# Kernel tuning notes

Hardware: AMD Instinct MI355X
Metric: run time of the kernel (lower is better)

## Reference

```python
import jax, jax.numpy as jnp
import numpy as np

B, L, V, E, H, DH, M, NL, BS, NR = 4, 2048, 32000, 512, 8, 64, 2048, 4, 64, 3
NEG = -1e9


def _sinusoidal_pe(length, dim):
    # LRA common_layers sinusoidal init: first half sin, second half cos.
    pos = np.arange(length, dtype=np.float32)[:, None]
    half = dim // 2
    div = np.exp(np.arange(half, dtype=np.float32) * -(np.log(10000.0) / half))
    pe = np.zeros((length, dim), np.float32)
    pe[:, :half] = np.sin(pos * div)
    pe[:, half:2 * half] = np.cos(pos * div)
    return jnp.asarray(pe)


def _bigbird_block_mask(seq_len, block_size, num_rand, seed):
    # BigBird sparsity at block granularity: window(3-band) + global(first/last
    # block rows & cols) + num_rand random blocks per row (connectivity_seed).
    nb = seq_len // block_size
    m = np.zeros((nb, nb), dtype=bool)
    for i in range(nb):
        for d in (-1, 0, 1):
            j = i + d
            if 0 <= j < nb:
                m[i, j] = True
    m[0, :] = True
    m[-1, :] = True
    m[:, 0] = True
    m[:, -1] = True
    rng = np.random.RandomState(seed)
    for i in range(1, nb - 1):
        avoid = {0, nb - 1, i - 1, i, i + 1}
        cand = np.array([j for j in range(nb) if j not in avoid])
        pick = rng.permutation(cand)[:num_rand]
        m[i, pick] = True
    return jnp.asarray(np.kron(m, np.ones((block_size, block_size), dtype=bool)))


_SPARSE_MASKS = [_bigbird_block_mask(L, BS, NR, lyr) for lyr in range(NL)]  # [L,L] bool per layer
_PE = _sinusoidal_pe(L, E)


def _ln(x, scale, bias, eps=1e-6):
    mu = jnp.mean(x, axis=-1, keepdims=True)
    var = jnp.mean(jnp.square(x - mu), axis=-1, keepdims=True)
    return (x - mu) * jax.lax.rsqrt(var + eps) * scale + bias


def setup_inputs() -> dict:
    key = jax.random.key(0)
    ks = jax.random.split(key, 12)
    s_qkv = 1.0 / np.sqrt(E)
    s_mlp = 1.0 / np.sqrt(E)
    return {
        "tokens": jax.random.randint(ks[0], (B, L), 0, V, dtype=jnp.int32),
        "embed": jax.random.normal(ks[1], (V, E), jnp.float32),
        "ln1_s": jnp.ones((NL, E), jnp.float32),
        "ln1_b": jnp.zeros((NL, E), jnp.float32),
        "wq": jax.random.normal(ks[2], (NL, E, H, DH), jnp.float32) * s_qkv,
        "wk": jax.random.normal(ks[3], (NL, E, H, DH), jnp.float32) * s_qkv,
        "wv": jax.random.normal(ks[4], (NL, E, H, DH), jnp.float32) * s_qkv,
        "wo": jax.random.normal(ks[5], (NL, H, DH, E), jnp.float32) * s_qkv,
        "ln2_s": jnp.ones((NL, E), jnp.float32),
        "ln2_b": jnp.zeros((NL, E), jnp.float32),
        "w1": jax.random.normal(ks[6], (NL, E, M), jnp.float32) * s_mlp,
        "b1": jnp.zeros((NL, M), jnp.float32),
        "w2": jax.random.normal(ks[7], (NL, M, E), jnp.float32) * (1.0 / np.sqrt(M)),
        "b2": jnp.zeros((NL, E), jnp.float32),
        "lnf_s": jnp.ones((E,), jnp.float32),
        "lnf_b": jnp.zeros((E,), jnp.float32),
    }


def reference(tokens, embed, ln1_s, ln1_b, wq, wk, wv, wo,
              ln2_s, ln2_b, w1, b1, w2, b2, lnf_s, lnf_b):
    pad = tokens > 0                                  # [B,L]
    x = embed[tokens] + _PE[None]                     # [B,L,E]
    scale = 1.0 / jnp.sqrt(jnp.asarray(DH, x.dtype))
    for lyr in range(NL):
        y = _ln(x, ln1_s[lyr], ln1_b[lyr])
        q = jnp.einsum("ble,ehd->blhd", y, wq[lyr]) * scale
        k = jnp.einsum("ble,ehd->blhd", y, wk[lyr])
        v = jnp.einsum("ble,ehd->blhd", y, wv[lyr])
        scores = jnp.einsum("blhd,bmhd->bhlm", q, k)  # [B,H,L,L]
        mask = (_SPARSE_MASKS[lyr][None, None]
                & pad[:, None, :, None] & pad[:, None, None, :])
        probs = jax.nn.softmax(jnp.where(mask, scores, NEG), axis=-1)
        o = jnp.einsum("bhlm,bmhd->blhd", probs, v)
        x = x + jnp.einsum("blhd,hde->ble", o, wo[lyr])
        y = _ln(x, ln2_s[lyr], ln2_b[lyr])
        h = jax.nn.gelu(jnp.einsum("ble,em->blm", y, w1[lyr]) + b1[lyr])
        x = x + jnp.einsum("blm,me->ble", h, w2[lyr]) + b2[lyr]
    return _ln(x, lnf_s, lnf_b)
```

## Files before the change

### kernel.cpp

```cpp
#include <hip/hip_runtime.h>
#include <hip/hip_bf16.h>
#include <cmath>
#include <cstdint>
#include <cstddef>

#define B_   4
#define L_   2048
#define E_   512
#define H_   8
#define DH_  64
#define M_   2048
#define NL_  4
#define NB_  32
#define BS_  64
#define CH_  12

typedef short bf16x8 __attribute__((ext_vector_type(8)));
typedef short bf16x4 __attribute__((ext_vector_type(4)));
typedef float f32x4 __attribute__((ext_vector_type(4)));

__device__ __forceinline__ short f2bf(float f) {
    union { __hip_bfloat16 h; short s; } u;
    u.h = __float2bfloat16(f);
    return u.s;
}
__device__ __forceinline__ float bf2f(short s) {
    union { short s; __hip_bfloat16 h; } u;
    u.s = s;
    return __bfloat162float(u.h);
}

struct MaskTable { unsigned m[NL_][NB_]; };
struct CxMT { unsigned key[624]; int pos; };

constexpr unsigned cx_next(CxMT& st) {
    if (st.pos >= 624) {
        for (int i = 0; i < 624; ++i) {
            unsigned y = (st.key[i] & 0x80000000u) | (st.key[(i + 1) % 624] & 0x7fffffffu);
            st.key[i] = st.key[(i + 397) % 624] ^ (y >> 1) ^ ((y & 1u) ? 0x9908b0dfu : 0u);
        }
        st.pos = 0;
    }
    unsigned y = st.key[st.pos++];
    y ^= y >> 11;
    y ^= (y << 7) & 0x9d2c5680u;
    y ^= (y << 15) & 0xefc60000u;
    y ^= y >> 18;
    return y;
}
constexpr unsigned cx_interval(CxMT& st, unsigned maxv) {
    if (maxv == 0u) return 0u;
    unsigned mask = maxv;
    mask |= mask >> 1; mask |= mask >> 2; mask |= mask >> 4;
    mask |= mask >> 8; mask |= mask >> 16;
    unsigned v = cx_next(st) & mask;
    while (v > maxv) v = cx_next(st) & mask;
    return v;
}
constexpr MaskTable compute_masks() {
    MaskTable T{};
    for (int lyr = 0; lyr < NL_; ++lyr) {
        unsigned m[NB_] = {};
        for (int i = 0; i < NB_; ++i) {
            unsigned w = 1u << i;
            if (i > 0) w |= 1u << (i - 1);
            if (i < NB_ - 1) w |= 1u << (i + 1);
            w |= 1u | (1u << (NB_ - 1));
            m[i] = w;
        }
        m[0] = 0xffffffffu;
        m[NB_ - 1] = 0xffffffffu;
        CxMT st{};
        unsigned s = (unsigned)lyr;
        for (int i = 0; i < 624; ++i) {
            st.key[i] = s;
            s = 1812433253u * (s ^ (s >> 30)) + (unsigned)i + 1u;
        }
        st.pos = 624;
        for (int i = 1; i < NB_ - 1; ++i) {
            int cand[NB_] = {};
            int n = 0;
            for (int j = 0; j < NB_; ++j) {
                if (j == 0 || j == NB_ - 1 || j == i - 1 || j == i || j == i + 1) continue;
                cand[n++] = j;
            }
            for (int kk = n - 1; kk >= 1; --kk) {
                int jj = (int)cx_interval(st, (unsigned)kk);
                int tmp = cand[kk]; cand[kk] = cand[jj]; cand[jj] = tmp;
            }
            m[i] |= (1u << cand[0]) | (1u << cand[1]) | (1u << cand[2]);
        }
        for (int i = 0; i < NB_; ++i) T.m[lyr][i] = m[i];
    }
    return T;
}

struct WorkTable {
    int n_items[NL_];
    int n_cmb[NL_];
    unsigned char itm_qb[NL_][40];
    unsigned char itm_j0[NL_][40];
    unsigned char itm_jn[NL_][40];
    unsigned char itm_slot[NL_][40];
    unsigned char cmb_qb[NL_][8];
    unsigned char cmb_slot0[NL_][8];
    unsigned char cmb_nch[NL_][8];
    unsigned char jlist[NL_][NB_][NB_];
};

constexpr WorkTable compute_work() {
    WorkTable T{};
    MaskTable M = compute_masks();
    for (int lyr = 0; lyr < NL_; ++lyr) {
        int items = 0, slots = 0, ncmb = 0;
        for (int qb = 0; qb < NB_; ++qb) {
            int cnt = 0;
            for (int j = 0; j < NB_; ++j)
                if ((M.m[lyr][qb] >> j) & 1u)
                    T.jlist[lyr][qb][cnt++] = (unsigned char)j;
            int nch = (cnt + CH_ - 1) / CH_;
            if (nch == 1) {
                T.itm_qb[lyr][items] = (unsigned char)qb;
                T.itm_j0[lyr][items] = 0;
                T.itm_jn[lyr][items] = (unsigned char)cnt;
                T.itm_slot[lyr][items] = 0xFF;
                items++;
            } else {
                T.cmb_qb[lyr][ncmb] = (unsigned char)qb;
                T.cmb_slot0[lyr][ncmb] = (unsigned char)slots;
                T.cmb_nch[lyr][ncmb] = (unsigned char)nch;
                ncmb++;
                int base = cnt / nch, rem = cnt % nch, off = 0;
                for (int c = 0; c < nch; ++c) {
                    int cl = base + (c < rem ? 1 : 0);
                    T.itm_qb[lyr][items] = (unsigned char)qb;
                    T.itm_j0[lyr][items] = (unsigned char)off;
                    T.itm_jn[lyr][items] = (unsigned char)cl;
                    T.itm_slot[lyr][items] = (unsigned char)slots;
                    items++; slots++; off += cl;
                }
            }
        }
        T.n_items[lyr] = items;
        T.n_cmb[lyr] = ncmb;
    }
    return T;
}

static constexpr WorkTable WT_HOST = compute_work();
__constant__ WorkTable g_wt = compute_work();

__global__ __launch_bounds__(256) void embed_kernel(const int* __restrict__ tokens,
                                                    const float* __restrict__ embed,
                                                    float* __restrict__ x) {
    int idx = blockIdx.x * 256 + threadIdx.x;
    int l = idx >> 6;
    int e0 = (idx & 63) * 8;
    float pe[8];
    #pragma unroll
    for (int j = 0; j < 8; ++j) {
        int e = e0 + j;
        int jj = e & 255;
        float div = expf((float)jj * -0.03597789207717895f);
        float arg = (float)l * div;
        pe[j] = (e < 256) ? sinf(arg) : cosf(arg);
    }
    #pragma unroll
    for (int b = 0; b < B_; ++b) {
        int tok = tokens[b * L_ + l];
        const float* em = embed + (size_t)tok * E_ + e0;
        f32x4 v0 = *(const f32x4*)em;
        f32x4 v1 = *(const f32x4*)(em + 4);
        #pragma unroll
        for (int j = 0; j < 4; ++j) { v0[j] += pe[j]; v1[j] += pe[4 + j]; }
        float* xo = x + ((size_t)(b * L_ + l)) * E_ + e0;
        *(f32x4*)xo = v0;
        *(f32x4*)(xo + 4) = v1;
    }
}

template<int OUTBF>
__global__ __launch_bounds__(256) void ln_kernel(const float* __restrict__ x,
                                                 const float* __restrict__ gamma,
                                                 const float* __restrict__ beta,
                                                 void* __restrict__ yout) {
    int t = threadIdx.x;
    int lane = t & 63;
    int row = blockIdx.x * 4 + (t >> 6);
    const float* xr = x + (size_t)row * E_ + lane * 8;
    f32x4 a0 = *(const f32x4*)xr;
    f32x4 a1 = *(const f32x4*)(xr + 4);
    float s = a0[0] + a0[1] + a0[2] + a0[3] + a1[0] + a1[1] + a1[2] + a1[3];
    #pragma unroll
    for (int off = 1; off < 64; off <<= 1) s += __shfl_xor(s, off, 64);
    float mu = s * (1.0f / E_);
    float q = 0.0f;
    #pragma unroll
    for (int j = 0; j < 4; ++j) { float d = a0[j] - mu; q += d * d; }
    #pragma unroll
    for (int j = 0; j < 4; ++j) { float d = a1[j] - mu; q += d * d; }
    #pragma unroll
    for (int off = 1; off < 64; off <<= 1) q += __shfl_xor(q, off, 64);
    float rstd = rsqrtf(q * (1.0f / E_) + 1e-6f);
    f32x4 g0 = *(const f32x4*)(gamma + lane * 8);
    f32x4 g1 = *(const f32x4*)(gamma + lane * 8 + 4);
    f32x4 b0 = *(const f32x4*)(beta + lane * 8);
    f32x4 b1 = *(const f32x4*)(beta + lane * 8 + 4);
    float o[8];
    #pragma unroll
    for (int j = 0; j < 4; ++j) o[j] = (a0[j] - mu) * rstd * g0[j] + b0[j];
    #pragma unroll
    for (int j = 0; j < 4; ++j) o[4 + j] = (a1[j] - mu) * rstd * g1[j] + b1[j];
    if (OUTBF) {
        bf16x8 pk;
        #pragma unroll
        for (int j = 0; j < 8; ++j) pk[j] = f2bf(o[j]);
        *(bf16x8*)((short*)yout + (size_t)row * E_ + lane * 8) = pk;
    } else {
        float* yr = (float*)yout + (size_t)row * E_ + lane * 8;
        *(f32x4*)yr = f32x4{o[0], o[1], o[2], o[3]};
        *(f32x4*)(yr + 4) = f32x4{o[4], o[5], o[6], o[7]};
    }
}

__global__ __launch_bounds__(256) void convT_kernel(const float* __restrict__ W,
                                                    short* __restrict__ Wt,
                                                    int K, int N,
                                                    size_t wStride, size_t wtStride,
                                                    float scale) {
    __shared__ float Ts[64][65];
    const float* Wl = W + blockIdx.z * wStride;
    short* Wtl = Wt + blockIdx.z * wtStride;
    int n0 = blockIdx.x * 64, k0 = blockIdx.y * 64;
    int t = threadIdx.x;
    int c = t & 63, r0 = t >> 6;
    #pragma unroll
    for (int i = 0; i < 16; ++i) {
        int r = r0 * 16 + i;
        Ts[r][c] = Wl[(size_t)(k0 + r) * N + n0 + c] * scale;
    }
    __syncthreads();
    #pragma unroll
    for (int i = 0; i < 16; ++i) {
        int r = r0 * 16 + i;
        Wtl[(size_t)(n0 + r) * K + k0 + c] = f2bf(Ts[c][r]);
    }
}

__device__ __forceinline__ float gelu_tanh(float x) {
    float u = x * (1.5957691216057308f + 0.07135480122394604f * x * x);
    return x / (1.0f + __expf(-u));
}

template<int BM, int BN, int ACT, int OUTBF>
__global__ __launch_bounds__(512) void mgemm_kernel(const short* __restrict__ A,
                                                    const short* __restrict__ Bt,
                                                    const float* __restrict__ bias,
                                                    const float* __restrict__ res,
                                                    void* __restrict__ Cout,
                                                    int M, int N, int K) {
    constexpr int WR = 2, WC = 4;
    constexpr int FM = BM / WR / 16;
    constexpr int FN = BN / WC / 16;
    constexpr int ASZ = BM * 64;
    constexpr int BSZ = BN * 64;
    constexpr int PAD = 8;
    constexpr int CW = BN + PAD;
    static_assert((size_t)(OUTBF ? BM * CW * 2 : BM * CW * 4) <= (size_t)2 * (ASZ + BSZ) * 2,
                  "epilogue stage must fit in dbuf LDS");
    __shared__ __align__(16) short smem[2 * (ASZ + BSZ)];

    int t = threadIdx.x;
    int w = t >> 6, l = t & 63;
    int l15 = l & 15, lg = l >> 4;
    int wr = w >> 2, wc = w & 3;
    int rowbase = wr * (BM / WR), colbase = wc * (BN / WC);

    int nwg = (int)(gridDim.x * gridDim.y);
    int orig = (int)(blockIdx.y * gridDim.x + blockIdx.x);
    int sid = (orig & 7) * (nwg >> 3) + (orig >> 3);
    int bx = sid % (int)gridDim.x, by = sid / (int)gridDim.x;
    int brow = by * BM, bcol = bx * BN;

    int swz = ((t & 7) ^ ((t >> 3) & 7)) * 8;
    f32x4 acc[FM][FN] = {};

    const int nt = K >> 6;

    auto stage = [&](int buf, int k0) {
        short* Ad = smem + buf * ASZ;
        short* Bd = smem + 2 * ASZ + buf * BSZ;
        #pragma unroll
        for (int it = 0; it < BM / 64; ++it) {
            int row = it * 64 + (t >> 3);
            const short* ga = A + (size_t)(brow + row) * K + k0 + swz;
            __builtin_amdgcn_global_load_lds(
                (const __attribute__((address_space(1))) unsigned int*)ga,
                (__attribute__((address_space(3))) unsigned int*)(Ad + (it * 64 + w * 8) * 64),
                16, 0, 0);
        }
        #pragma unroll
        for (int it = 0; it < BN / 64; ++it) {
            int row = it * 64 + (t >> 3);
            const short* gb = Bt + (size_t)(bcol + row) * K + k0 + swz;
            __builtin_amdgcn_global_load_lds(
                (const __attribute__((address_space(1))) unsigned int*)gb,
                (__attribute__((address_space(3))) unsigned int*)(Bd + (it * 64 + w * 8) * 64),
                16, 0, 0);
        }
    };

    stage(0, 0);
    asm volatile("s_waitcnt vmcnt(0)" ::: "memory");
    __builtin_amdgcn_s_barrier();

    int cur = 0;
    for (int kt = 0; kt < nt; ++kt) {
        if (kt + 1 < nt) stage(cur ^ 1, (kt + 1) << 6);
        const short* Ar = smem + cur * ASZ;
        const short* Br = smem + 2 * ASZ + cur * BSZ;
        #pragma unroll
        for (int kk = 0; kk < 64; kk += 32) {
            bf16x8 af[FM], bfr[FN];
            #pragma unroll
            for (int m = 0; m < FM; ++m)
                af[m] = *(const bf16x8*)(Ar + (rowbase + m * 16 + l15) * 64
                                            + (((kk >> 3) + lg) ^ (l15 & 7)) * 8);
            #pragma unroll
            for (int n = 0; n < FN; ++n)
                bfr[n] = *(const bf16x8*)(Br + (colbase + n * 16 + l15) * 64
                                             + (((kk >> 3) + lg) ^ (l15 & 7)) * 8);
            #pragma unroll
            for (int m = 0; m < FM; ++m)
                #pragma unroll
                for (int n = 0; n < FN; ++n)
                    acc[m][n] = __builtin_amdgcn_mfma_f32_16x16x32_bf16(af[m], bfr[n], acc[m][n], 0, 0, 0);
        }
        asm volatile("s_waitcnt vmcnt(0) lgkmcnt(0)" ::: "memory");
        __builtin_amdgcn_s_barrier();
        cur ^= 1;
    }

    if (OUTBF) {
        short* Cs = smem;
        #pragma unroll
        for (int m = 0; m < FM; ++m) {
            int row = rowbase + m * 16 + lg * 4;
            #pragma unroll
            for (int n = 0; n < FN; ++n) {
                int col = colbase + n * 16 + l15;
                float bv = bias ? bias[bcol + col] : 0.0f;
                #pragma unroll
                for (int r = 0; r < 4; ++r) {
                    float vv = acc[m][n][r] + bv;
                    if (ACT == 1) vv = gelu_tanh(vv);
                    Cs[(row + r) * CW + col] = f2bf(vv);
                }
            }
        }
        __syncthreads();
        #pragma unroll
        for (int it = 0; it < BM * BN / 8 / 512; ++it) {
            int c = it * 512 + t;
            int row = c / (BN / 8), c8 = c % (BN / 8);
            *(bf16x8*)((short*)Cout + (size_t)(brow + row) * N + bcol + c8 * 8) =
                *(const bf16x8*)(Cs + row * CW + c8 * 8);
        }
    } else {
        float* Cs = (float*)smem;
        #pragma unroll
        for (int m = 0; m < FM; ++m) {
            int row = rowbase + m * 16 + lg * 4;
            #pragma unroll
            for (int n = 0; n < FN; ++n) {
                int col = colbase + n * 16 + l15;
                float bv = bias ? bias[bcol + col] : 0.0f;
                #pragma unroll
                for (int r = 0; r < 4; ++r)
                    Cs[(row + r) * CW + col] = acc[m][n][r] + bv;
            }
        }
        __syncthreads();
        #pragma unroll
        for (int it = 0; it < BM * BN / 4 / 512; ++it) {
            int c = it * 512 + t;
            int row = c / (BN / 4), c4 = c % (BN / 4);
            f32x4 vv = *(const f32x4*)(Cs + row * CW + c4 * 4);
            size_t gi = (size_t)(brow + row) * N + bcol + c4 * 4;
            if (res) vv += *(const f32x4*)(res + gi);
            *(f32x4*)((float*)Cout + gi) = vv;
        }
    }
}

#define KSTR 72

__global__ __launch_bounds__(256) void attn_kernel(const short* __restrict__ qkv,
                                                   const int* __restrict__ tokens,
                                                   short* __restrict__ o,
                                                   float* __restrict__ pacc,
                                                   float* __restrict__ pm,
                                                   float* __restrict__ pl,
                                                   int lyr) {
    __shared__ __align__(16) short Ks[64][KSTR];
    __shared__ __align__(16) short Vt[64][KSTR];
    __shared__ __align__(16) short Pw[4][16][KSTR];
    __shared__ unsigned long long qbits_s;
    __shared__ unsigned long long kbits_s;

    int item = blockIdx.x, h = blockIdx.y, b = blockIdx.z;
    int qb   = g_wt.itm_qb[lyr][item];
    int j0   = g_wt.itm_j0[lyr][item];
    int jn   = g_wt.itm_jn[lyr][item];
    int slot = g_wt.itm_slot[lyr][item];
    const unsigned char* jl = g_wt.jlist[lyr][qb];

    int t = threadIdx.x;
    int l = t & 63, w = t >> 6;
    int l15 = l & 15, lg = l >> 4;
    int srow = t >> 3, sdb = t & 7;

    if (t < 64) {
        unsigned long long qm = __ballot(tokens[b * L_ + qb * 64 + t] > 0);
        if (t == 0) qbits_s = qm;
    }

    int qrow = qb * 64 + w * 16 + l15;
    const short* qp = qkv + (size_t)(b * L_ + qrow) * 1536 + h * 64;
    bf16x8 qf0 = *(const bf16x8*)(qp + lg * 8);
    bf16x8 qf1 = *(const bf16x8*)(qp + lg * 8 + 32);

    f32x4 acc[4] = {};
    float m_r = -INFINITY, l_r = 0.0f;

    bf16x8 kr0, kr1, vr0, vr1;
    int pn = 0;
    auto LOAD = [&](int ci) {
        int jb = jl[j0 + ci];
        const short* base = qkv + (size_t)(b * L_ + jb * 64 + srow) * 1536 + h * 64;
        kr0 = *(const bf16x8*)(base + 512 + sdb * 8);
        kr1 = *(const bf16x8*)(base + (size_t)32 * 1536 + 512 + sdb * 8);
        vr0 = *(const bf16x8*)(base + 1024 + sdb * 8);
        vr1 = *(const bf16x8*)(base + (size_t)32 * 1536 + 1024 + sdb * 8);
        if (t < 64) pn = tokens[b * L_ + jb * 64 + t];
    };
    LOAD(0);

    for (int ci = 0; ci < jn; ++ci) {
        __syncthreads();
        *(bf16x8*)&Ks[srow][sdb * 8] = kr0;
        *(bf16x8*)&Ks[srow + 32][sdb * 8] = kr1;
        #pragma unroll
        for (int j = 0; j < 8; ++j) {
            Vt[sdb * 8 + j][(srow & 7) + 8 * ((srow >> 3) ^ sdb)] = vr0[j];
            Vt[sdb * 8 + j][(srow & 7) + 8 * (((srow >> 3) + 4) ^ sdb)] = vr1[j];
        }
        if (t < 64) {
            unsigned long long km = __ballot(pn > 0);
            if (t == 0) kbits_s = km;
        }
        __syncthreads();

        if (ci + 1 < jn) LOAD(ci + 1);

        f32x4 sacc[4];
        __builtin_amdgcn_s_setprio(1);
        #pragma unroll
        for (int f = 0; f < 4; ++f) {
            bf16x8 kk0 = *(const bf16x8*)&Ks[16 * f + l15][lg * 8];
            bf16x8 kk1 = *(const bf16x8*)&Ks[16 * f + l15][lg * 8 + 32];
            f32x4 z = {};
            z = __builtin_amdgcn_mfma_f32_16x16x32_bf16(kk0, qf0, z, 0, 0, 0);
            z = __builtin_amdgcn_mfma_f32_16x16x32_bf16(kk1, qf1, z, 0, 0, 0);
            sacc[f] = z;
        }
        __builtin_amdgcn_s_setprio(0);

        unsigned long long kb = kbits_s;
        bool pq = (qbits_s >> (w * 16 + l15)) & 1ull;
        unsigned vm = 0;
        #pragma unroll
        for (int f = 0; f < 4; ++f)
            vm |= ((unsigned)(kb >> (16 * f + 4 * lg)) & 0xFu) << (4 * f);
        if (!pq) vm = 0;

        float mx = -INFINITY;
        #pragma unroll
        for (int f = 0; f < 4; ++f)
            #pragma unroll
            for (int r = 0; r < 4; ++r)
                if ((vm >> (4 * f + r)) & 1u) mx = fmaxf(mx, sacc[f][r]);
        mx = fmaxf(mx, __shfl_xor(mx, 16, 64));
        mx = fmaxf(mx, __shfl_xor(mx, 32, 64));
        float nm = fmaxf(m_r, mx);

        float pv[16];
        float sum = 0.0f;
        #pragma unroll
        for (int f = 0; f < 4; ++f)
            #pragma unroll
            for (int r = 0; r < 4; ++r) {
                float p = ((vm >> (4 * f + r)) & 1u) ? __expf(sacc[f][r] - nm) : 0.0f;
                pv[4 * f + r] = p;
                sum += p;
            }
        sum += __shfl_xor(sum, 16, 64);
        sum += __shfl_xor(sum, 32, 64);
        float al = (nm == -INFINITY) ? 1.0f : __expf(m_r - nm);
        m_r = nm;
        l_r = l_r * al + sum;

        #pragma unroll
        for (int f = 0; f < 4; ++f) {
            bf16x4 pk;
            #pragma unroll
            for (int r = 0; r < 4; ++r) pk[r] = f2bf(pv[4 * f + r]);
            *(bf16x4*)&Pw[w][l15][16 * f + 4 * lg] = pk;
        }

        float alr[4];
        #pragma unroll
        for (int r = 0; r < 4; ++r) alr[r] = __shfl(al, lg * 4 + r, 64);
        #pragma unroll
        for (int fd = 0; fd < 4; ++fd)
            #pragma unroll
            for (int r = 0; r < 4; ++r) acc[fd][r] *= alr[r];

        bf16x8 pa0 = *(const bf16x8*)&Pw[w][l15][lg * 8];
        bf16x8 pa1 = *(const bf16x8*)&Pw[w][l15][lg * 8 + 32];
        __builtin_amdgcn_s_setprio(1);
        #pragma unroll
        for (int fd = 0; fd < 4; ++fd) {
            int dd = 16 * fd + l15;
            bf16x8 vv0 = *(const bf16x8*)&Vt[dd][8 * (lg ^ (dd >> 3))];
            bf16x8 vv1 = *(const bf16x8*)&Vt[dd][8 * ((4 + lg) ^ (dd >> 3))];
            acc[fd] = __builtin_amdgcn_mfma_f32_16x16x32_bf16(pa0, vv0, acc[fd], 0, 0, 0);
            acc[fd] = __builtin_amdgcn_mfma_f32_16x16x32_bf16(pa1, vv1, acc[fd], 0, 0, 0);
        }
        __builtin_amdgcn_s_setprio(0);
    }

    float lrr[4], mrr[4];
    #pragma unroll
    for (int r = 0; r < 4; ++r) {
        lrr[r] = __shfl(l_r, lg * 4 + r, 64);
        mrr[r] = __shfl(m_r, lg * 4 + r, 64);
    }
    unsigned long long qbits = qbits_s;

    if (slot == 0xFF) {
        #pragma unroll
        for (int r = 0; r < 4; ++r) {
            int rw = lg * 4 + r;
            int gl = qb * 64 + w * 16 + rw;
            size_t ob = (size_t)(b * L_ + gl) * 512 + h * 64 + l15;
            bool ok = ((qbits >> (w * 16 + rw)) & 1ull) && (lrr[r] > 0.0f);
            if (ok) {
                float inv = 1.0f / lrr[r];
                #pragma unroll
                for (int fd = 0; fd < 4; ++fd) o[ob + 16 * fd] = f2bf(acc[fd][r] * inv);
            } else {
                #pragma unroll
                for (int fd = 0; fd < 4; ++fd) {
                    float s = 0.0f;
                    for (int m = 0; m < L_; ++m)
                        s += bf2f(qkv[(size_t)(b * L_ + m) * 1536 + 1024 + h * 64 + 16 * fd + l15]);
                    o[ob + 16 * fd] = f2bf(s * (1.0f / L_));
                }
            }
        }
    } else {
        size_t pb = ((size_t)slot * B_ + b) * H_ + h;
        #pragma unroll
        for (int r = 0; r < 4; ++r) {
            int rloc = w * 16 + lg * 4 + r;
            #pragma unroll
            for (int fd = 0; fd < 4; ++fd)
                pacc[pb * 4096 + (size_t)rloc * 64 + 16 * fd + l15] = acc[fd][r];
            if (l15 == 0) {
                pm[pb * 64 + rloc] = mrr[r];
                pl[pb * 64 + rloc] = lrr[r];
            }
        }
    }
}

__global__ __launch_bounds__(256) void attn_combine(const short* __restrict__ qkv,
                                                    const int* __restrict__ tokens,
                                                    short* __restrict__ o,
                                                    const float* __restrict__ pacc,
                                                    const float* __restrict__ pm,
                                                    const float* __restrict__ pl,
                                                    int lyr) {
    int ci = blockIdx.x, h = blockIdx.y, b = blockIdx.z;
    int qb  = g_wt.cmb_qb[lyr][ci];
    int s0  = g_wt.cmb_slot0[lyr][ci];
    int nch = g_wt.cmb_nch[lyr][ci];
    int t = threadIdx.x;
    int r = t >> 2, dq = t & 3;
    int grow = qb * 64 + r;
    bool pq = tokens[b * L_ + grow] > 0;
    float M = -INFINITY;
    for (int c = 0; c < nch; ++c)
        M = fmaxf(M, pm[(((size_t)(s0 + c) * B_ + b) * H_ + h) * 64 + r]);
    size_t ob = (size_t)(b * L_ + grow) * 512 + h * 64 + dq * 16;
    if (pq && M > -1e30f) {
        float lsum = 0.0f;
        float accd[16] = {};
        for (int c = 0; c < nch; ++c) {
            size_t pb = ((size_t)(s0 + c) * B_ + b) * H_ + h;
            float wgt = __expf(pm[pb * 64 + r] - M);
            lsum += pl[pb * 64 + r] * wgt;
            const float* pa = pacc + pb * 4096 + (size_t)r * 64 + dq * 16;
            #pragma unroll
            for (int j = 0; j < 16; ++j) accd[j] += pa[j] * wgt;
        }
        float inv = 1.0f / lsum;
        #pragma unroll
        for (int j = 0; j < 16; ++j) o[ob + j] = f2bf(accd[j] * inv);
    } else {
        #pragma unroll
        for (int j = 0; j < 16; ++j) {
            float s = 0.0f;
            for (int m = 0; m < L_; ++m)
                s += bf2f(qkv[(size_t)(b * L_ + m) * 1536 + 1024 + h * 64 + dq * 16 + j]);
            o[ob + j] = f2bf(s * (1.0f / L_));
        }
    }
}

extern "C" void kernel_launch(void* const* d_in, const int* in_sizes, int n_in,
                              void* d_out, int out_size, void* d_ws, size_t ws_size,
                              hipStream_t stream) {
    (void)in_sizes; (void)n_in; (void)out_size; (void)ws_size;
    const int*   tokens = (const int*)d_in[0];
    const float* embed  = (const float*)d_in[1];
    const float* ln1_s  = (const float*)d_in[2];
    const float* ln1_b  = (const float*)d_in[3];
    const float* wq     = (const float*)d_in[4];
    const float* wk     = (const float*)d_in[5];
    const float* wv     = (const float*)d_in[6];
    const float* wo     = (const float*)d_in[7];
    const float* ln2_s  = (const float*)d_in[8];
    const float* ln2_b  = (const float*)d_in[9];
    const float* w1     = (const float*)d_in[10];
    const float* b1     = (const float*)d_in[11];
    const float* w2     = (const float*)d_in[12];
    const float* b2     = (const float*)d_in[13];
    const float* lnf_s  = (const float*)d_in[14];
    const float* lnf_b  = (const float*)d_in[15];
    float* out = (float*)d_out;

    const size_t BLE = (size_t)B_ * L_ * E_;
    char* ws = (char*)d_ws;
    float* x    = (float*)ws;
    short* yb   = (short*)(x + BLE);
    short* R    = yb + BLE;
    short* qkv  = R;
    short* ob   = R + 3 * BLE;
    short* hb   = R;
    short* qkvt = R + 4 * BLE;
    short* wot  = qkvt + (size_t)NL_ * 1536 * 512;
    short* w1t  = wot + (size_t)NL_ * 512 * 512;
    short* w2t  = w1t + (size_t)NL_ * 2048 * 512;
    float* pacc = (float*)(w2t + (size_t)NL_ * 512 * 2048);
    float* pm   = pacc + (size_t)8 * B_ * H_ * 4096;
    float* pl   = pm + (size_t)8 * B_ * H_ * 64;

    convT_kernel<<<dim3(8, 8, NL_), 256, 0, stream>>>(wq, qkvt,          512, 512, 262144, 786432, 0.125f);
    convT_kernel<<<dim3(8, 8, NL_), 256, 0, stream>>>(wk, qkvt + 262144, 512, 512, 262144, 786432, 1.0f);
    convT_kernel<<<dim3(8, 8, NL_), 256, 0, stream>>>(wv, qkvt + 524288, 512, 512, 262144, 786432, 1.0f);
    convT_kernel<<<dim3(8, 8, NL_), 256, 0, stream>>>(wo, wot,           512, 512, 262144, 262144, 1.0f);
    convT_kernel<<<dim3(32, 8, NL_), 256, 0, stream>>>(w1, w1t,          512, 2048, 1048576, 1048576, 1.0f);
    convT_kernel<<<dim3(8, 32, NL_), 256, 0, stream>>>(w2, w2t,          2048, 512, 1048576, 1048576, 1.0f);

    embed_kernel<<<(L_ * E_ / 8) / 256, 256, 0, stream>>>(tokens, embed, x);

    const int MR = B_ * L_;
    const int LNG = MR / 4;
    for (int lyr = 0; lyr < NL_; ++lyr) {
        ln_kernel<1><<<LNG, 256, 0, stream>>>(x, ln1_s + lyr * E_, ln1_b + lyr * E_, yb);
        mgemm_kernel<128, 128, 0, 1><<<dim3(12, 64), 512, 0, stream>>>(
            yb, qkvt + (size_t)lyr * 786432, nullptr, nullptr, qkv, MR, 1536, 512);
        attn_kernel<<<dim3(WT_HOST.n_items[lyr], H_, B_), 256, 0, stream>>>(
            qkv, tokens, ob, pacc, pm, pl, lyr);
        attn_combine<<<dim3(WT_HOST.n_cmb[lyr], H_, B_), 256, 0, stream>>>(
            qkv, tokens, ob, pacc, pm, pl, lyr);
        mgemm_kernel<64, 128, 0, 0><<<dim3(4, 128), 512, 0, stream>>>(
            ob, wot + (size_t)lyr * 262144, nullptr, x, x, MR, 512, 512);
        ln_kernel<1><<<LNG, 256, 0, stream>>>(x, ln2_s + lyr * E_, ln2_b + lyr * E_, yb);
        mgemm_kernel<128, 128, 1, 1><<<dim3(16, 64), 512, 0, stream>>>(
            yb, w1t + (size_t)lyr * 1048576, b1 + (size_t)lyr * M_, nullptr, hb, MR, 2048, 512);
        mgemm_kernel<64, 128, 0, 0><<<dim3(4, 128), 512, 0, stream>>>(
            hb, w2t + (size_t)lyr * 1048576, b2 + (size_t)lyr * E_, x, x, MR, 512, 2048);
    }
    ln_kernel<0><<<LNG, 256, 0, stream>>>(x, lnf_s, lnf_b, out);
}
```

Baseline: 602.3 us.

## Double-buffer K/V shared tiles in sparse attention and shrink key chunk size

The attention kernel now keeps two LDS buffers for K, V and the key pad bits. The next block is stored into the spare buffer after the current compute, so each iteration needs one barrier instead of two, and global loads are issued two blocks ahead. The key-chunk size CH_ drops from 12 to 8, which splits query rows into more work items and raises grid parallelism, at the cost of more partial-result combining. LDS use roughly doubles for K/V, which may lower occupancy.

New measurement: 594.5 us. No clear change (-1.3%).

```diff
diff --git a/kernel.cpp b/kernel.cpp
--- a/kernel.cpp
+++ b/kernel.cpp
@@ -13,7 +13,7 @@
 #define NL_  4
 #define NB_  32
 #define BS_  64
-#define CH_  12
+#define CH_  8
 
 typedef short bf16x8 __attribute__((ext_vector_type(8)));
 typedef short bf16x4 __attribute__((ext_vector_type(4)));
@@ -98,10 +98,10 @@
 struct WorkTable {
     int n_items[NL_];
     int n_cmb[NL_];
-    unsigned char itm_qb[NL_][40];
-    unsigned char itm_j0[NL_][40];
-    unsigned char itm_jn[NL_][40];
-    unsigned char itm_slot[NL_][40];
+    unsigned char itm_qb[NL_][48];
+    unsigned char itm_j0[NL_][48];
+    unsigned char itm_jn[NL_][48];
+    unsigned char itm_slot[NL_][48];
     unsigned char cmb_qb[NL_][8];
     unsigned char cmb_slot0[NL_][8];
     unsigned char cmb_nch[NL_][8];
@@ -402,11 +402,11 @@
                                                    float* __restrict__ pm,
                                                    float* __restrict__ pl,
                                                    int lyr) {
-    __shared__ __align__(16) short Ks[64][KSTR];
-    __shared__ __align__(16) short Vt[64][KSTR];
+    __shared__ __align__(16) short Ks[2][64][KSTR];
+    __shared__ __align__(16) short Vt[2][64][KSTR];
     __shared__ __align__(16) short Pw[4][16][KSTR];
     __shared__ unsigned long long qbits_s;
-    __shared__ unsigned long long kbits_s;
+    __shared__ unsigned long long kbits_s[2];
 
     int item = blockIdx.x, h = blockIdx.y, b = blockIdx.z;
     int qb   = g_wt.itm_qb[lyr][item];
@@ -444,31 +444,33 @@
         vr1 = *(const bf16x8*)(base + (size_t)32 * 1536 + 1024 + sdb * 8);
         if (t < 64) pn = tokens[b * L_ + jb * 64 + t];
     };
-    LOAD(0);
-
-    for (int ci = 0; ci < jn; ++ci) {
-        __syncthreads();
-        *(bf16x8*)&Ks[srow][sdb * 8] = kr0;
-        *(bf16x8*)&Ks[srow + 32][sdb * 8] = kr1;
+    auto STORE = [&](int buf) {
+        *(bf16x8*)&Ks[buf][srow][sdb * 8] = kr0;
+        *(bf16x8*)&Ks[buf][srow + 32][sdb * 8] = kr1;
         #pragma unroll
         for (int j = 0; j < 8; ++j) {
-            Vt[sdb * 8 + j][(srow & 7) + 8 * ((srow >> 3) ^ sdb)] = vr0[j];
-            Vt[sdb * 8 + j][(srow & 7) + 8 * (((srow >> 3) + 4) ^ sdb)] = vr1[j];
+            Vt[buf][sdb * 8 + j][(srow & 7) + 8 * ((srow >> 3) ^ sdb)] = vr0[j];
+            Vt[buf][sdb * 8 + j][(srow & 7) + 8 * (((srow >> 3) + 4) ^ sdb)] = vr1[j];
         }
         if (t < 64) {
             unsigned long long km = __ballot(pn > 0);
-            if (t == 0) kbits_s = km;
-        }
-        __syncthreads();
-
-        if (ci + 1 < jn) LOAD(ci + 1);
-
+            if (t == 0) kbits_s[buf] = km;
+        }
+    };
+
+    LOAD(0);
+    STORE(0);
+    if (jn > 1) LOAD(1);
+    __syncthreads();
+
+    int cur = 0;
+    for (int ci = 0; ci < jn; ++ci) {
         f32x4 sacc[4];
         __builtin_amdgcn_s_setprio(1);
         #pragma unroll
         for (int f = 0; f < 4; ++f) {
-            bf16x8 kk0 = *(const bf16x8*)&Ks[16 * f + l15][lg * 8];
-            bf16x8 kk1 = *(const bf16x8*)&Ks[16 * f + l15][lg * 8 + 32];
+            bf16x8 kk0 = *(const bf16x8*)&Ks[cur][16 * f + l15][lg * 8];
+            bf16x8 kk1 = *(const bf16x8*)&Ks[cur][16 * f + l15][lg * 8 + 32];
             f32x4 z = {};
             z = __builtin_amdgcn_mfma_f32_16x16x32_bf16(kk0, qf0, z, 0, 0, 0);
             z = __builtin_amdgcn_mfma_f32_16x16x32_bf16(kk1, qf1, z, 0, 0, 0);
@@ -476,7 +478,7 @@
         }
         __builtin_amdgcn_s_setprio(0);
 
-        unsigned long long kb = kbits_s;
+        unsigned long long kb = kbits_s[cur];
         bool pq = (qbits_s >> (w * 16 + l15)) & 1ull;
         unsigned vm = 0;
         #pragma unroll
@@ -532,12 +534,19 @@
         #pragma unroll
         for (int fd = 0; fd < 4; ++fd) {
             int dd = 16 * fd + l15;
-            bf16x8 vv0 = *(const bf16x8*)&Vt[dd][8 * (lg ^ (dd >> 3))];
-            bf16x8 vv1 = *(const bf16x8*)&Vt[dd][8 * ((4 + lg) ^ (dd >> 3))];
+            bf16x8 vv0 = *(const bf16x8*)&Vt[cur][dd][8 * (lg ^ (dd >> 3))];
+            bf16x8 vv1 = *(const bf16x8*)&Vt[cur][dd][8 * ((4 + lg) ^ (dd >> 3))];
             acc[fd] = __builtin_amdgcn_mfma_f32_16x16x32_bf16(pa0, vv0, acc[fd], 0, 0, 0);
             acc[fd] = __builtin_amdgcn_mfma_f32_16x16x32_bf16(pa1, vv1, acc[fd], 0, 0, 0);
         }
         __builtin_amdgcn_s_setprio(0);
+
+        if (ci + 1 < jn) {
+            STORE(cur ^ 1);
+            if (ci + 2 < jn) LOAD(ci + 2);
+        }
+        __syncthreads();
+        cur ^= 1;
     }
 
     float lrr[4], mrr[4];
```
